# Kernel tuning notes

Hardware: AMD Instinct MI355X
Metric: run time of the kernel (lower is better)

The kernel has to match this reference:

```python
import jax, jax.numpy as jnp
import numpy as np

N_NODES = 50000
N_EDGES = 800000
N_REL = 3
N_GRAPHS = 500
EMB = 128
IN_DIM = EMB * 3
HID = 256
N_CLASS = 10
N_SHAPE, N_COLOR, MAX_POS = 8, 8, 128


def rgcn_layer(h, src, dst, etype, W, root, b):
    """PyG RGCNConv with default aggr='mean':
    out[v] = sum_r mean_{(j->v) in E_r} h[j] @ W[r] + h[v] @ root + b
    Aggregate raw features per (dst, relation) bucket, then apply relation matmuls.
    """
    N, R = h.shape[0], W.shape[0]
    seg = dst * R + etype  # combined (node, relation) segment id
    sums = jax.ops.segment_sum(h[src], seg, num_segments=N * R)          # (N*R, d)
    cnt = jax.ops.segment_sum(jnp.ones(seg.shape, h.dtype), seg, num_segments=N * R)
    mean = (sums / jnp.maximum(cnt, 1.0)[:, None]).reshape(N, R, -1)     # (N, R, d)
    return jnp.einsum('nrd,rdh->nh', mean, W) + h @ root + b


def setup_inputs() -> dict:
    key = jax.random.key(0)
    ks = jax.random.split(key, 20)
    f32 = jnp.float32
    inp = {
        's': jax.random.randint(ks[0], (N_NODES,), 0, N_SHAPE),
        'c': jax.random.randint(ks[1], (N_NODES,), 0, N_COLOR),
        'p': jax.random.randint(ks[2], (N_NODES,), 0, MAX_POS),
        'edge_index': jax.random.randint(ks[3], (2, N_EDGES), 0, N_NODES),
        'edge_type': jax.random.randint(ks[4], (N_EDGES,), 0, N_REL),
        'batch': jnp.sort(jax.random.randint(ks[5], (N_NODES,), 0, N_GRAPHS)),
        'shape_emb': jax.random.normal(ks[6], (N_SHAPE, EMB), f32),
        'color_emb': jax.random.normal(ks[7], (N_COLOR, EMB), f32),
        'pos_emb': jax.random.normal(ks[8], (MAX_POS, EMB), f32),
        'W1': jax.random.normal(ks[9], (N_REL, IN_DIM, HID), f32) / np.sqrt(IN_DIM),
        'root1': jax.random.normal(ks[10], (IN_DIM, HID), f32) / np.sqrt(IN_DIM),
        'b1': jnp.zeros((HID,), f32),
        'W2': jax.random.normal(ks[11], (N_REL, HID, HID), f32) / np.sqrt(HID),
        'root2': jax.random.normal(ks[12], (HID, HID), f32) / np.sqrt(HID),
        'b2': jnp.zeros((HID,), f32),
        'lin_w': jax.random.normal(ks[13], (HID, N_CLASS), f32) / np.sqrt(HID),
        'lin_b': jnp.zeros((N_CLASS,), f32),
    }
    return inp


def reference(s, c, p, edge_index, edge_type, batch,
              shape_emb, color_emb, pos_emb,
              W1, root1, b1, W2, root2, b2, lin_w, lin_b):
    src, dst = edge_index[0], edge_index[1]
    h = jnp.concatenate([shape_emb[s], color_emb[c], pos_emb[p]], axis=-1)  # (N, 3*emb)
    h = jax.nn.relu(rgcn_layer(h, src, dst, edge_type, W1, root1, b1))
    h = jax.nn.relu(rgcn_layer(h, src, dst, edge_type, W2, root2, b2))
    # global_mean_pool over graphs
    gsum = jax.ops.segment_sum(h, batch, num_segments=N_GRAPHS)
    gcnt = jax.ops.segment_sum(jnp.ones((h.shape[0],), h.dtype), batch, num_segments=N_GRAPHS)
    pooled = gsum / jnp.maximum(gcnt, 1.0)[:, None]
    return pooled @ lin_w + lin_b
```

## Files before the change

kernel.cpp:

```cpp
#include <hip/hip_runtime.h>
#include <hip/hip_bf16.h>

#define NN 50000
#define NE 800000
#define NR 3
#define NG 500
#define NB (NN * NR)
#define NCLS 10
#define NCMB 8192
#define CHUNK 2048
#define NBLK ((NB + CHUNK - 1) / CHUNK)

#define P1_COMBO   196
#define P1_ZCNT    586
#define P1_ZPOOL   502
#define P1_TAB     576
#define P1_WF      1024
#define P1_TOTAL   (P1_COMBO + P1_ZCNT + P1_ZPOOL + P1_TAB + P1_WF)
#define P2_CNT     3125
#define P2_TB      768
#define P2_TOTAL   (P2_CNT + P2_TB)

typedef __hip_bfloat16 bf16;
typedef __attribute__((ext_vector_type(8))) short short8;
typedef __attribute__((ext_vector_type(4))) short shortx4;
typedef __attribute__((ext_vector_type(4))) float floatx4;

static __device__ __forceinline__ float b2f(bf16 x) { return __bfloat162float(x); }
static __device__ __forceinline__ bf16  f2b(float x) { return __float2bfloat16(x); }
static __device__ __forceinline__ float bs2f(short x) {
    return __bfloat162float(*reinterpret_cast<const bf16*>(&x));
}
static __device__ __forceinline__ short f2bs(float x) {
    bf16 b = __float2bfloat16(x);
    return *reinterpret_cast<const short*>(&b);
}
static __device__ __forceinline__ int rfl(int x) {
    return __builtin_amdgcn_readfirstlane(x);
}

__global__ __launch_bounds__(256) void prep1(const int* __restrict__ s,
                                             const int* __restrict__ c,
                                             const int* __restrict__ p,
                                             const float* __restrict__ se,
                                             const float* __restrict__ ce,
                                             const float* __restrict__ pe,
                                             const float* __restrict__ W1,
                                             const float* __restrict__ root1,
                                             const float* __restrict__ W2,
                                             const float* __restrict__ root2,
                                             int* __restrict__ combo,
                                             unsigned* __restrict__ cnt,
                                             unsigned* __restrict__ poolz,
                                             float* __restrict__ tab,
                                             bf16* __restrict__ Wf) {
    int b = blockIdx.x, t = threadIdx.x;
    if (b < P1_COMBO) {
        int n = b * 256 + t;
        if (n < NN) combo[n] = (s[n] << 10) | (c[n] << 7) | p[n];
        return;
    }
    b -= P1_COMBO;
    if (b < P1_ZCNT) {
        int i = b * 256 + t;
        if (i < NB) cnt[i] = 0u;
        return;
    }
    b -= P1_ZCNT;
    if (b < P1_ZPOOL) {
        int i = b * 256 + t;
        if (i < NG * 256 + NG) poolz[i] = 0u;
        return;
    }
    b -= P1_ZPOOL;
    if (b < P1_TAB) {
        int r = b / 144, row = b % 144;
        const float* A; int segk;
        if (row < 8)       { A = se + row * 128;        segk = 0; }
        else if (row < 16) { A = ce + (row - 8) * 128;  segk = 128; }
        else               { A = pe + (row - 16) * 128; segk = 256; }
        const float* W = (r < 3) ? (W1 + (size_t)r * 384 * 256) : root1;
        float acc = 0.f;
        for (int k = 0; k < 128; ++k)
            acc += A[k] * W[(size_t)(segk + k) * 256 + t];
        tab[((size_t)r * 144 + row) * 256 + t] = acc;
        return;
    }
    b -= P1_TAB;
    {
        int idx = b * 256 + t;
        int j     = idx & 7;
        int lane  = (idx >> 3) & 63;
        int ni    = (idx >> 9) & 3;
        int chunk = (idx >> 11) & 31;
        int colblk = idx >> 16;
        int col = colblk * 64 + ni * 16 + (lane & 15);
        int k   = chunk * 32 + (lane >> 4) * 8 + j;
        float v = (k < 768) ? W2[((size_t)(k >> 8) * 256 + (k & 255)) * 256 + col]
                            : root2[(size_t)(k - 768) * 256 + col];
        Wf[idx] = f2b(v);
    }
}

__global__ __launch_bounds__(256) void prep2(const int* __restrict__ ei,
                                             const int* __restrict__ et,
                                             int* __restrict__ cnt,
                                             const float* __restrict__ tab,
                                             const float* __restrict__ b1,
                                             bf16* __restrict__ tb2) {
    int b = blockIdx.x, t = threadIdx.x;
    if (b < P2_CNT) {
        int e = b * 256 + t;
        if (e < NE) atomicAdd(&cnt[ei[NE + e] * NR + et[e]], 1);
        return;
    }
    b -= P2_CNT;
    if (b < 256) {
        int r = b >> 6, sc = b & 63, si = sc >> 3, ci = sc & 7;
        float v = tab[((size_t)r * 144 + si) * 256 + t]
                + tab[((size_t)r * 144 + 8 + ci) * 256 + t];
        if (r == 3) v += b1[t];
        tb2[(size_t)b * 256 + t] = f2b(v);
    } else {
        int bb = b - 256;
        int r = bb >> 7, pi = bb & 127;
        tb2[(size_t)(256 + bb) * 256 + t] =
            f2b(tab[((size_t)r * 144 + 16 + pi) * 256 + t]);
    }
}

__global__ __launch_bounds__(256) void scan_block_sums(const int* __restrict__ cnt,
                                                       int* __restrict__ bsum) {
    __shared__ int sm[256];
    int b = blockIdx.x, t = threadIdx.x;
    int base = b * CHUNK + t * 8, s = 0;
#pragma unroll
    for (int j = 0; j < 8; ++j) { int i = base + j; if (i < NB) s += cnt[i]; }
    sm[t] = s; __syncthreads();
    for (int st = 128; st; st >>= 1) { if (t < st) sm[t] += sm[t + st]; __syncthreads(); }
    if (!t) bsum[b] = sm[0];
}

__global__ __launch_bounds__(256) void scan_write(const int* __restrict__ cnt,
                                                  const int* __restrict__ bsum,
                                                  int* __restrict__ off,
                                                  int* __restrict__ cursor) {
    int b = blockIdx.x, t = threadIdx.x;
    int bbase = 0;
    for (int i = 0; i < b; ++i) bbase += bsum[i];
    if (b == 0 && t == 0) {
        int tot = 0;
        for (int i = 0; i < NBLK; ++i) tot += bsum[i];
        off[NB] = tot;
    }
    int base = b * CHUNK + t * 8;
    int v[8], ts = 0;
#pragma unroll
    for (int j = 0; j < 8; ++j) { int i = base + j; v[j] = (i < NB) ? cnt[i] : 0; ts += v[j]; }
    int lane = t & 63, wv = t >> 6;
    int incl = ts;
    for (int d = 1; d < 64; d <<= 1) {
        int o = __shfl_up(incl, d, 64);
        if (lane >= d) incl += o;
    }
    __shared__ int wsum[4];
    if (lane == 63) wsum[wv] = incl;
    __syncthreads();
    int wbase = 0;
    for (int w = 0; w < wv; ++w) wbase += wsum[w];
    int run = bbase + wbase + incl - ts;
#pragma unroll
    for (int j = 0; j < 8; ++j) {
        int i = base + j;
        if (i < NB) { off[i] = run; cursor[i] = run; }
        run += v[j];
    }
}

__global__ __launch_bounds__(256) void scatter_edges(const int* __restrict__ ei,
                                                     const int* __restrict__ et,
                                                     const int* __restrict__ combo,
                                                     int* __restrict__ cursor,
                                                     unsigned* __restrict__ esc) {
    int e = blockIdx.x * 256 + threadIdx.x;
    if (e >= NE) return;
    int b = ei[NE + e] * NR + et[e];
    int pos = atomicAdd(&cursor[b], 1);
    int s = ei[e];
    esc[pos] = ((unsigned)s << 13) | (unsigned)combo[s];
}

__global__ __launch_bounds__(256, 4) void l1_fused(const int* __restrict__ off,
                                                   const unsigned* __restrict__ esc,
                                                   const int* __restrict__ combo,
                                                   const bf16* __restrict__ tb2,
                                                   bf16* __restrict__ h1) {
    int wave = threadIdx.x >> 6, lane = threadIdx.x & 63;
    int dst = blockIdx.x * 4 + wave;
    if (dst >= NN) return;
    int l4 = lane * 4;
    int b0 = dst * NR;
    int o0 = rfl(off[b0]),     o1 = rfl(off[b0 + 1]),
        o2 = rfl(off[b0 + 2]), o3 = rfl(off[b0 + 3]);
    float inv0 = (o1 > o0) ? 1.f / (float)(o1 - o0) : 0.f;
    float inv1 = (o2 > o1) ? 1.f / (float)(o2 - o1) : 0.f;
    float inv2 = (o3 > o2) ? 1.f / (float)(o3 - o2) : 0.f;
    int cmbD = rfl(combo[dst]);
    shortx4 rsc = *(const shortx4*)(tb2 + (size_t)(192 + (cmbD >> 7)) * 256 + l4);
    shortx4 rp  = *(const shortx4*)(tb2 + (size_t)(640 + (cmbD & 127)) * 256 + l4);
    float s[4];
#pragma unroll
    for (int i = 0; i < 4; ++i) s[i] = bs2f(rsc[i]) + bs2f(rp[i]);

    for (int jb = o0; jb < o3; jb += 8) {
        shortx4 sc[8], sp[8]; float w[8];
#pragma unroll
        for (int q = 0; q < 8; ++q) {
            int k = jb + q;
            bool g = k < o3;
            int kk = g ? k : o0;
            unsigned e = esc[kk];
            int r = (kk >= o1) + (kk >= o2);
            w[q] = g ? ((k >= o2) ? inv2 : ((k >= o1) ? inv1 : inv0)) : 0.f;
            sc[q] = *(const shortx4*)(tb2 + (size_t)(r * 64 + ((e & 8191) >> 7)) * 256 + l4);
            sp[q] = *(const shortx4*)(tb2 + (size_t)(256 + r * 128 + (e & 127)) * 256 + l4);
        }
#pragma unroll
        for (int q = 0; q < 8; ++q)
#pragma unroll
            for (int i = 0; i < 4; ++i)
                s[i] += (bs2f(sc[q][i]) + bs2f(sp[q][i])) * w[q];
    }
    shortx4 o;
#pragma unroll
    for (int i = 0; i < 4; ++i) o[i] = f2bs(fmaxf(s[i], 0.f));
    *(shortx4*)(h1 + (size_t)dst * 256 + l4) = o;
}

__global__ __launch_bounds__(256, 4) void agg_all(const int* __restrict__ off,
                                                  const unsigned* __restrict__ esc,
                                                  const bf16* __restrict__ h1,
                                                  bf16* __restrict__ hagg) {
    int wave = threadIdx.x >> 6, lane = threadIdx.x & 63;
    int dst = blockIdx.x * 4 + wave;
    if (dst >= NN) return;
    int l4 = lane * 4;
    int b0 = dst * NR;
    int o0 = rfl(off[b0]),     o1 = rfl(off[b0 + 1]),
        o2 = rfl(off[b0 + 2]), o3 = rfl(off[b0 + 3]);
    float s0[4] = {}, s1[4] = {}, s2[4] = {};
    int n = max(o1 - o0, max(o2 - o1, o3 - o2));
    for (int k = 0; k < n; k += 4) {
#pragma unroll
        for (int kk = 0; kk < 4; ++kk) {
            int i0 = o0 + k + kk, i1 = o1 + k + kk, i2 = o2 + k + kk;
            bool g0 = i0 < o1, g1 = i1 < o2, g2 = i2 < o3;
            unsigned e0 = esc[g0 ? i0 : 0];
            unsigned e1 = esc[g1 ? i1 : 0];
            unsigned e2 = esc[g2 ? i2 : 0];
            shortx4 v0 = *(const shortx4*)(h1 + (size_t)(g0 ? (e0 >> 13) : 0) * 256 + l4);
            shortx4 v1 = *(const shortx4*)(h1 + (size_t)(g1 ? (e1 >> 13) : 0) * 256 + l4);
            shortx4 v2 = *(const shortx4*)(h1 + (size_t)(g2 ? (e2 >> 13) : 0) * 256 + l4);
            float m0 = g0 ? 1.f : 0.f, m1 = g1 ? 1.f : 0.f, m2 = g2 ? 1.f : 0.f;
#pragma unroll
            for (int i = 0; i < 4; ++i) {
                s0[i] += bs2f(v0[i]) * m0;
                s1[i] += bs2f(v1[i]) * m1;
                s2[i] += bs2f(v2[i]) * m2;
            }
        }
    }
    float inv0 = (o1 > o0) ? 1.f / (float)(o1 - o0) : 0.f;
    float inv1 = (o2 > o1) ? 1.f / (float)(o2 - o1) : 0.f;
    float inv2 = (o3 > o2) ? 1.f / (float)(o3 - o2) : 0.f;
    shortx4 w0, w1, w2;
#pragma unroll
    for (int i = 0; i < 4; ++i) {
        w0[i] = f2bs(s0[i] * inv0);
        w1[i] = f2bs(s1[i] * inv1);
        w2[i] = f2bs(s2[i] * inv2);
    }
    bf16* hd = hagg + (size_t)dst * 768 + l4;
    *(shortx4*)(hd)       = w0;
    *(shortx4*)(hd + 256) = w1;
    *(shortx4*)(hd + 512) = w2;
}

__global__ __launch_bounds__(256) void gemm_cat(const bf16* __restrict__ hagg,
                                                const bf16* __restrict__ h1,
                                                const bf16* __restrict__ Wf,
                                                const float* __restrict__ bias,
                                                const int* __restrict__ batch,
                                                float* __restrict__ pool,
                                                float* __restrict__ gcnt) {
    __shared__ short lds[4][2][32 * 40];
    const int t = threadIdx.x;
    const int wave = t >> 6, lane = t & 63;
    const int quad = lane >> 4, l16 = lane & 15;
    const int row0 = blockIdx.x * 32;
    const int colblk = wave;
    const int rsub = lane >> 2;
    const int ksub = (lane & 3) * 8;
    short* A0 = lds[wave][0];
    short* A1 = lds[wave][1];

    const int r0 = min(row0 + rsub, NN - 1);
    const int r1 = min(row0 + 16 + rsub, NN - 1);
    const bf16* gA0 = hagg + (size_t)r0 * 768 + ksub;
    const bf16* gA1 = hagg + (size_t)r1 * 768 + ksub;
    const bf16* gH0 = h1 + (size_t)r0 * 256 + ksub;
    const bf16* gH1 = h1 + (size_t)r1 * 256 + ksub;
    const short8* bbase = (const short8*)Wf + (size_t)colblk * 32 * 4 * 64 + lane;

    auto loadA2 = [&](int k0, short8& a0, short8& a1) {
        if (k0 < 768) { a0 = *(const short8*)(gA0 + k0); a1 = *(const short8*)(gA1 + k0); }
        else          { a0 = *(const short8*)(gH0 + k0 - 768); a1 = *(const short8*)(gH1 + k0 - 768); }
    };
    auto loadB = [&](int chunk, short8* bf4) {
        const short8* bp = bbase + (size_t)chunk * 4 * 64;
#pragma unroll
        for (int ni = 0; ni < 4; ++ni) bf4[ni] = bp[ni * 64];
    };

    floatx4 acc[2][4] = {};
    short8 aE0, aE1, bE[4];
    short8 aO0, aO1, bO[4];
    loadA2(0, aE0, aE1);  loadB(0, bE);
    loadA2(32, aO0, aO1); loadB(1, bO);

#pragma unroll
    for (int i = 0; i < 32; i += 2) {
        *(short8*)&A0[rsub * 40 + ksub] = aE0;
        *(short8*)&A0[(16 + rsub) * 40 + ksub] = aE1;
        {
            short8 af0 = *(const short8*)&A0[l16 * 40 + quad * 8];
            short8 af1 = *(const short8*)&A0[(16 + l16) * 40 + quad * 8];
#pragma unroll
            for (int ni = 0; ni < 4; ++ni) {
                acc[0][ni] = __builtin_amdgcn_mfma_f32_16x16x32_bf16(af0, bE[ni], acc[0][ni], 0, 0, 0);
                acc[1][ni] = __builtin_amdgcn_mfma_f32_16x16x32_bf16(af1, bE[ni], acc[1][ni], 0, 0, 0);
            }
        }
        if (i + 2 < 32) { loadA2((i + 2) * 32, aE0, aE1); loadB(i + 2, bE); }
        *(short8*)&A1[rsub * 40 + ksub] = aO0;
        *(short8*)&A1[(16 + rsub) * 40 + ksub] = aO1;
        {
            short8 af0 = *(const short8*)&A1[l16 * 40 + quad * 8];
            short8 af1 = *(const short8*)&A1[(16 + l16) * 40 + quad * 8];
#pragma unroll
            for (int ni = 0; ni < 4; ++ni) {
                acc[0][ni] = __builtin_amdgcn_mfma_f32_16x16x32_bf16(af0, bO[ni], acc[0][ni], 0, 0, 0);
                acc[1][ni] = __builtin_amdgcn_mfma_f32_16x16x32_bf16(af1, bO[ni], acc[1][ni], 0, 0, 0);
            }
        }
        if (i + 3 < 32) { loadA2((i + 3) * 32, aO0, aO1); loadB(i + 3, bO); }
    }

    __syncthreads();
    short* st = &lds[0][0][0];
#pragma unroll
    for (int mi = 0; mi < 2; ++mi) {
#pragma unroll
        for (int ni = 0; ni < 4; ++ni) {
            int n = colblk * 64 + ni * 16 + l16;
            float bn = bias[n];
#pragma unroll
            for (int ii = 0; ii < 4; ++ii) {
                int lrow = mi * 16 + quad * 4 + ii;
                float v = (row0 + lrow < NN) ? fmaxf(acc[mi][ni][ii] + bn, 0.f) : 0.f;
                st[lrow * 260 + n] = f2bs(v);
            }
        }
    }
    __syncthreads();
    int nrows = NN - row0; if (nrows > 32) nrows = 32;
    int curg = batch[row0];
    float a = 0.f, cntf = 0.f;
    for (int rr = 0; rr < nrows; ++rr) {
        int g = batch[row0 + rr];
        if (g != curg) {
            atomicAdd(&pool[(size_t)curg * 256 + t], a);
            if (t == 0) atomicAdd(&gcnt[curg], cntf);
            a = 0.f; cntf = 0.f; curg = g;
        }
        a += bs2f(st[rr * 260 + t]);
        cntf += 1.f;
    }
    atomicAdd(&pool[(size_t)curg * 256 + t], a);
    if (t == 0) atomicAdd(&gcnt[curg], cntf);
}

__global__ __launch_bounds__(256) void final_head(const float* __restrict__ pool,
                                                  const float* __restrict__ gcnt,
                                                  const float* __restrict__ lin_w,
                                                  const float* __restrict__ lin_b,
                                                  float* __restrict__ out) {
    __shared__ float sm[256];
    int g = blockIdx.x, t = threadIdx.x;
    float inv = 1.0f / fmaxf(gcnt[g], 1.0f);
    sm[t] = pool[(size_t)g * 256 + t] * inv;
    __syncthreads();
    if (t < NCLS) {
        float s = lin_b[t];
        for (int d = 0; d < 256; ++d) s += sm[d] * lin_w[d * NCLS + t];
        out[g * NCLS + t] = s;
    }
}

extern "C" void kernel_launch(void* const* d_in, const int* in_sizes, int n_in,
                              void* d_out, int out_size, void* d_ws, size_t ws_size,
                              hipStream_t stream) {
    const int*   s_idx = (const int*)d_in[0];
    const int*   c_idx = (const int*)d_in[1];
    const int*   p_idx = (const int*)d_in[2];
    const int*   ei    = (const int*)d_in[3];
    const int*   et    = (const int*)d_in[4];
    const int*   batch = (const int*)d_in[5];
    const float* se    = (const float*)d_in[6];
    const float* ce    = (const float*)d_in[7];
    const float* pe    = (const float*)d_in[8];
    const float* W1    = (const float*)d_in[9];
    const float* root1 = (const float*)d_in[10];
    const float* b1    = (const float*)d_in[11];
    const float* W2    = (const float*)d_in[12];
    const float* root2 = (const float*)d_in[13];
    const float* b2    = (const float*)d_in[14];
    const float* lin_w = (const float*)d_in[15];
    const float* lin_b = (const float*)d_in[16];
    float* out = (float*)d_out;

    char* w = (char*)d_ws;
    size_t o = 0;
    auto alloc = [&](size_t bytes) -> void* {
        o = (o + 15) & ~(size_t)15;
        void* ptr = w + o;
        o += bytes;
        return ptr;
    };
    bf16*     hagg   = (bf16*)    alloc((size_t)NN * 768 * 2);
    bf16*     h1     = (bf16*)    alloc((size_t)NN * 256 * 2);
    bf16*     tb2    = (bf16*)    alloc((size_t)768 * 256 * 2);
    int*      combo  = (int*)     alloc((size_t)NN * 4);
    unsigned* esc    = (unsigned*)alloc((size_t)NE * 4);
    int*      cnt    = (int*)     alloc((size_t)NB * 4);
    int*      off    = (int*)     alloc((size_t)(NB + 1) * 4);
    int*      cursor = (int*)     alloc((size_t)NB * 4);
    int*      bsum   = (int*)     alloc((size_t)NBLK * 4);
    float*    tab    = (float*)   alloc((size_t)4 * 144 * 256 * 4);
    bf16*     Wf     = (bf16*)    alloc((size_t)256 * 1024 * 2);
    float*    pool   = (float*)   alloc((size_t)NG * 256 * 4);
    float*    gcnt   = (float*)   alloc((size_t)NG * 4);
    (void)ws_size;

    prep1<<<P1_TOTAL, 256, 0, stream>>>(s_idx, c_idx, p_idx, se, ce, pe,
                                        W1, root1, W2, root2,
                                        combo, (unsigned*)cnt, (unsigned*)pool, tab, Wf);
    prep2<<<P2_TOTAL, 256, 0, stream>>>(ei, et, cnt, tab, b1, tb2);
    scan_block_sums<<<NBLK, 256, 0, stream>>>(cnt, bsum);
    scan_write<<<NBLK, 256, 0, stream>>>(cnt, bsum, off, cursor);
    scatter_edges<<<(NE + 255) / 256, 256, 0, stream>>>(ei, et, combo, cursor, esc);
    l1_fused<<<(NN + 3) / 4, 256, 0, stream>>>(off, esc, combo, tb2, h1);
    agg_all<<<(NN + 3) / 4, 256, 0, stream>>>(off, esc, h1, hagg);
    gemm_cat<<<(NN + 31) / 32, 256, 0, stream>>>(hagg, h1, Wf, b2, batch, pool, gcnt);
    final_head<<<NG, 256, 0, stream>>>(pool, gcnt, lin_w, lin_b, out);
}
```

Baseline: 375.4 us.

## Stage layer-1 lookup table slices in LDS and split edges across quarter-waves

Replaces the per-destination layer-1 kernel with one that loads a 64-column slice of the precomputed relation/embedding table (576 rows) into shared memory per block. Each block then handles 128 destinations for one column slice, and the four 16-lane groups of a wave process different edges in parallel before a shuffle reduction. The aim is to turn scattered global/L2 table reads into LDS reads. The cost is a table load per block, LDS capacity limiting occupancy, and edge indices being re-read by four slice blocks.

```diff
diff --git a/kernel.cpp b/kernel.cpp
--- a/kernel.cpp
+++ b/kernel.cpp
@@ -20,6 +20,12 @@
 #define P2_CNT     3125
 #define P2_TB      768
 #define P2_TOTAL   (P2_CNT + P2_TB)
+
+#define L1_DPB     128
+#define L1_DPW     32
+#define L1_ROWS    576
+#define L1_STRIDE  68
+#define L1_CHUNKS  ((NN + L1_DPB - 1) / L1_DPB)
 
 typedef __hip_bfloat16 bf16;
 typedef __attribute__((ext_vector_type(8))) short short8;
@@ -190,51 +196,74 @@
     esc[pos] = ((unsigned)s << 13) | (unsigned)combo[s];
 }
 
-__global__ __launch_bounds__(256, 4) void l1_fused(const int* __restrict__ off,
-                                                   const unsigned* __restrict__ esc,
-                                                   const int* __restrict__ combo,
-                                                   const bf16* __restrict__ tb2,
-                                                   bf16* __restrict__ h1) {
-    int wave = threadIdx.x >> 6, lane = threadIdx.x & 63;
-    int dst = blockIdx.x * 4 + wave;
-    if (dst >= NN) return;
-    int l4 = lane * 4;
-    int b0 = dst * NR;
-    int o0 = rfl(off[b0]),     o1 = rfl(off[b0 + 1]),
-        o2 = rfl(off[b0 + 2]), o3 = rfl(off[b0 + 3]);
-    float inv0 = (o1 > o0) ? 1.f / (float)(o1 - o0) : 0.f;
-    float inv1 = (o2 > o1) ? 1.f / (float)(o2 - o1) : 0.f;
-    float inv2 = (o3 > o2) ? 1.f / (float)(o3 - o2) : 0.f;
-    int cmbD = rfl(combo[dst]);
-    shortx4 rsc = *(const shortx4*)(tb2 + (size_t)(192 + (cmbD >> 7)) * 256 + l4);
-    shortx4 rp  = *(const shortx4*)(tb2 + (size_t)(640 + (cmbD & 127)) * 256 + l4);
-    float s[4];
-#pragma unroll
-    for (int i = 0; i < 4; ++i) s[i] = bs2f(rsc[i]) + bs2f(rp[i]);
-
-    for (int jb = o0; jb < o3; jb += 8) {
-        shortx4 sc[8], sp[8]; float w[8];
-#pragma unroll
-        for (int q = 0; q < 8; ++q) {
-            int k = jb + q;
-            bool g = k < o3;
-            int kk = g ? k : o0;
-            unsigned e = esc[kk];
-            int r = (kk >= o1) + (kk >= o2);
-            w[q] = g ? ((k >= o2) ? inv2 : ((k >= o1) ? inv1 : inv0)) : 0.f;
-            sc[q] = *(const shortx4*)(tb2 + (size_t)(r * 64 + ((e & 8191) >> 7)) * 256 + l4);
-            sp[q] = *(const shortx4*)(tb2 + (size_t)(256 + r * 128 + (e & 127)) * 256 + l4);
-        }
-#pragma unroll
-        for (int q = 0; q < 8; ++q)
+__global__ __launch_bounds__(256) void l1_lds(const int* __restrict__ off,
+                                              const unsigned* __restrict__ esc,
+                                              const int* __restrict__ combo,
+                                              const bf16* __restrict__ tb2,
+                                              bf16* __restrict__ h1) {
+    __shared__ short T[L1_ROWS * L1_STRIDE];
+    const int slice = blockIdx.x & 3;
+    const int chunk = blockIdx.x >> 2;
+    const int t = threadIdx.x;
+
+    for (int i = t; i < L1_ROWS * 16; i += 256) {
+        int row = i >> 4, c = i & 15;
+        int grow = (row < 192) ? row : row + 64;
+        *(shortx4*)&T[row * L1_STRIDE + c * 4] =
+            *(const shortx4*)(tb2 + (size_t)grow * 256 + slice * 64 + c * 4);
+    }
+    __syncthreads();
+
+    const int wave = t >> 6, lane = t & 63;
+    const int q = lane >> 4, l16 = lane & 15;
+    const int dst0 = chunk * L1_DPB + wave * L1_DPW;
+    const int myd = slice * 64 + l16 * 4;
+
+    for (int di = 0; di < L1_DPW; ++di) {
+        int dst = dst0 + di;
+        if (dst >= NN) break;
+        int b0 = dst * NR;
+        int o0 = rfl(off[b0]),     o1 = rfl(off[b0 + 1]),
+            o2 = rfl(off[b0 + 2]), o3 = rfl(off[b0 + 3]);
+        float inv0 = (o1 > o0) ? 1.f / (float)(o1 - o0) : 0.f;
+        float inv1 = (o2 > o1) ? 1.f / (float)(o2 - o1) : 0.f;
+        float inv2 = (o3 > o2) ? 1.f / (float)(o3 - o2) : 0.f;
+        float acc[4] = {};
+        for (int jb = o0; jb < o3; jb += 8) {
+            int ka = jb + q, kb = jb + 4 + q;
+            bool ga = ka < o3, gb = kb < o3;
+            int kka = ga ? ka : o0, kkb = gb ? kb : o0;
+            unsigned ea = esc[kka];
+            unsigned eb = esc[kkb];
+            int ra = (kka >= o1) + (kka >= o2);
+            int rb = (kkb >= o1) + (kkb >= o2);
+            float wa = ga ? ((ka >= o2) ? inv2 : ((ka >= o1) ? inv1 : inv0)) : 0.f;
+            float wb = gb ? ((kb >= o2) ? inv2 : ((kb >= o1) ? inv1 : inv0)) : 0.f;
+            shortx4 sa = *(const shortx4*)&T[(ra * 64 + ((ea & 8191u) >> 7)) * L1_STRIDE + l16 * 4];
+            shortx4 pa = *(const shortx4*)&T[(192 + ra * 128 + (int)(ea & 127u)) * L1_STRIDE + l16 * 4];
+            shortx4 sb = *(const shortx4*)&T[(rb * 64 + ((eb & 8191u) >> 7)) * L1_STRIDE + l16 * 4];
+            shortx4 pb = *(const shortx4*)&T[(192 + rb * 128 + (int)(eb & 127u)) * L1_STRIDE + l16 * 4];
 #pragma unroll
             for (int i = 0; i < 4; ++i)
-                s[i] += (bs2f(sc[q][i]) + bs2f(sp[q][i])) * w[q];
-    }
-    shortx4 o;
-#pragma unroll
-    for (int i = 0; i < 4; ++i) o[i] = f2bs(fmaxf(s[i], 0.f));
-    *(shortx4*)(h1 + (size_t)dst * 256 + l4) = o;
+                acc[i] += (bs2f(sa[i]) + bs2f(pa[i])) * wa
+                        + (bs2f(sb[i]) + bs2f(pb[i])) * wb;
+        }
+#pragma unroll
+        for (int i = 0; i < 4; ++i) {
+            acc[i] += __shfl_xor(acc[i], 16);
+            acc[i] += __shfl_xor(acc[i], 32);
+        }
+        if (q == 0) {
+            int cmbD = rfl(combo[dst]);
+            shortx4 rsc = *(const shortx4*)(tb2 + (size_t)(192 + (cmbD >> 7)) * 256 + myd);
+            shortx4 rp  = *(const shortx4*)(tb2 + (size_t)(640 + (cmbD & 127)) * 256 + myd);
+            shortx4 o;
+#pragma unroll
+            for (int i = 0; i < 4; ++i)
+                o[i] = f2bs(fmaxf(acc[i] + bs2f(rsc[i]) + bs2f(rp[i]), 0.f));
+            *(shortx4*)(h1 + (size_t)dst * 256 + myd) = o;
+        }
+    }
 }
 
 __global__ __launch_bounds__(256, 4) void agg_all(const int* __restrict__ off,
@@ -459,7 +488,7 @@
     scan_block_sums<<<NBLK, 256, 0, stream>>>(cnt, bsum);
     scan_write<<<NBLK, 256, 0, stream>>>(cnt, bsum, off, cursor);
     scatter_edges<<<(NE + 255) / 256, 256, 0, stream>>>(ei, et, combo, cursor, esc);
-    l1_fused<<<(NN + 3) / 4, 256, 0, stream>>>(off, esc, combo, tb2, h1);
+    l1_lds<<<L1_CHUNKS * 4, 256, 0, stream>>>(off, esc, combo, tb2, h1);
     agg_all<<<(NN + 3) / 4, 256, 0, stream>>>(off, esc, h1, hagg);
     gemm_cat<<<(NN + 31) / 32, 256, 0, stream>>>(hagg, h1, Wf, b2, batch, pool, gcnt);
     final_head<<<NG, 256, 0, stream>>>(pool, gcnt, lin_w, lin_b, out);
```

Measured after the change: 518.1 us. 38.0% more time.

## Compute layer-1 as per-node histogram times table via MFMA

Applied to the files above, without the earlier changes.

Layer 1 is rewritten so each block of 64 destination nodes first builds, in shared memory, a byte histogram of (relation, shape-color) and (relation, position) table indices from incoming edges. It then multiplies the mean-weighted histogram by the precomputed 768x256 table with bf16 MFMA instructions. This replaces per-edge gathers of 256-wide table rows with a dense small GEMM. A new prep3 kernel pre-swizzles the table into MFMA-friendly layout. Byte counters can overflow if more than 255 edges hit one bin, and the weights are now rounded to bf16 before the multiply.

```diff
diff --git a/kernel.cpp b/kernel.cpp
--- a/kernel.cpp
+++ b/kernel.cpp
@@ -20,6 +20,10 @@
 #define P2_CNT     3125
 #define P2_TB      768
 #define P2_TOTAL   (P2_CNT + P2_TB)
+
+#define L1_DPB     64
+#define L1_HS      776
+#define L1_BLOCKS  ((NN + L1_DPB - 1) / L1_DPB)
 
 typedef __hip_bfloat16 bf16;
 typedef __attribute__((ext_vector_type(8))) short short8;
@@ -129,6 +133,17 @@
     }
 }
 
+__global__ __launch_bounds__(256) void prep3(const bf16* __restrict__ tb2,
+                                             bf16* __restrict__ tbf) {
+    int idx = blockIdx.x * 256 + threadIdx.x;
+    int j = idx & 7, lane = (idx >> 3) & 63, ni = (idx >> 9) & 3;
+    int rest = idx >> 11;
+    int chunk = rest % 24, colblk = rest / 24;
+    int col = colblk * 64 + ni * 16 + (lane & 15);
+    int k   = chunk * 32 + (lane >> 4) * 8 + j;
+    tbf[idx] = tb2[(size_t)k * 256 + col];
+}
+
 __global__ __launch_bounds__(256) void scan_block_sums(const int* __restrict__ cnt,
                                                        int* __restrict__ bsum) {
     __shared__ int sm[256];
@@ -190,51 +205,108 @@
     esc[pos] = ((unsigned)s << 13) | (unsigned)combo[s];
 }
 
-__global__ __launch_bounds__(256, 4) void l1_fused(const int* __restrict__ off,
-                                                   const unsigned* __restrict__ esc,
-                                                   const int* __restrict__ combo,
-                                                   const bf16* __restrict__ tb2,
-                                                   bf16* __restrict__ h1) {
-    int wave = threadIdx.x >> 6, lane = threadIdx.x & 63;
-    int dst = blockIdx.x * 4 + wave;
-    if (dst >= NN) return;
-    int l4 = lane * 4;
-    int b0 = dst * NR;
-    int o0 = rfl(off[b0]),     o1 = rfl(off[b0 + 1]),
-        o2 = rfl(off[b0 + 2]), o3 = rfl(off[b0 + 3]);
-    float inv0 = (o1 > o0) ? 1.f / (float)(o1 - o0) : 0.f;
-    float inv1 = (o2 > o1) ? 1.f / (float)(o2 - o1) : 0.f;
-    float inv2 = (o3 > o2) ? 1.f / (float)(o3 - o2) : 0.f;
-    int cmbD = rfl(combo[dst]);
-    shortx4 rsc = *(const shortx4*)(tb2 + (size_t)(192 + (cmbD >> 7)) * 256 + l4);
-    shortx4 rp  = *(const shortx4*)(tb2 + (size_t)(640 + (cmbD & 127)) * 256 + l4);
-    float s[4];
-#pragma unroll
-    for (int i = 0; i < 4; ++i) s[i] = bs2f(rsc[i]) + bs2f(rp[i]);
-
-    for (int jb = o0; jb < o3; jb += 8) {
-        shortx4 sc[8], sp[8]; float w[8];
-#pragma unroll
-        for (int q = 0; q < 8; ++q) {
-            int k = jb + q;
-            bool g = k < o3;
-            int kk = g ? k : o0;
-            unsigned e = esc[kk];
-            int r = (kk >= o1) + (kk >= o2);
-            w[q] = g ? ((k >= o2) ? inv2 : ((k >= o1) ? inv1 : inv0)) : 0.f;
-            sc[q] = *(const shortx4*)(tb2 + (size_t)(r * 64 + ((e & 8191) >> 7)) * 256 + l4);
-            sp[q] = *(const shortx4*)(tb2 + (size_t)(256 + r * 128 + (e & 127)) * 256 + l4);
-        }
-#pragma unroll
-        for (int q = 0; q < 8; ++q)
-#pragma unroll
-            for (int i = 0; i < 4; ++i)
-                s[i] += (bs2f(sc[q][i]) + bs2f(sp[q][i])) * w[q];
-    }
-    shortx4 o;
-#pragma unroll
-    for (int i = 0; i < 4; ++i) o[i] = f2bs(fmaxf(s[i], 0.f));
-    *(shortx4*)(h1 + (size_t)dst * 256 + l4) = o;
+__global__ __launch_bounds__(256) void l1_hist(const int* __restrict__ off,
+                                               const unsigned* __restrict__ esc,
+                                               const int* __restrict__ combo,
+                                               const bf16* __restrict__ tbf,
+                                               bf16* __restrict__ h1) {
+    __shared__ __align__(16) unsigned char HIST[L1_DPB * L1_HS];
+    __shared__ int SOFF[193];
+    __shared__ float INV[L1_DPB][4];
+    const int t = threadIdx.x;
+    const int dst0 = blockIdx.x * L1_DPB;
+
+    for (int i = t; i < (L1_DPB * L1_HS) / 4; i += 256)
+        ((unsigned*)HIST)[i] = 0u;
+    for (int i = t; i < 193; i += 256)
+        SOFF[i] = off[min(dst0 * NR + i, NB)];
+    __syncthreads();
+
+    if (t < L1_DPB) {
+        int base = 3 * t;
+#pragma unroll
+        for (int r = 0; r < 3; ++r) {
+            int c = SOFF[base + r + 1] - SOFF[base + r];
+            INV[t][r] = (c > 0) ? 1.f / (float)c : 0.f;
+        }
+        INV[t][3] = 1.f;
+        if (dst0 + t < NN) {
+            int c = combo[dst0 + t];
+            HIST[t * L1_HS + 192 + (c >> 7)] = 1;
+            HIST[t * L1_HS + 640 + (c & 127)] = 1;
+        }
+    }
+    int E0 = SOFF[0], E1 = SOFF[192];
+    for (int e = E0 + t; e < E1; e += 256) {
+        unsigned ev = esc[e];
+        int lo = 0, hi = 191;
+#pragma unroll 1
+        while (lo < hi) {
+            int mid = (lo + hi + 1) >> 1;
+            if (SOFF[mid] <= e) lo = mid; else hi = mid - 1;
+        }
+        int dr = lo / 3, rel = lo - dr * 3;
+        int sc = (int)((ev & 8191u) >> 7), p = (int)(ev & 127u);
+        int a1 = dr * L1_HS + rel * 64 + sc;
+        int a2 = dr * L1_HS + 256 + rel * 128 + p;
+        atomicAdd((unsigned*)&HIST[a1 & ~3], 1u << (8 * (a1 & 3)));
+        atomicAdd((unsigned*)&HIST[a2 & ~3], 1u << (8 * (a2 & 3)));
+    }
+    __syncthreads();
+
+    const int wave = t >> 6, lane = t & 63;
+    const int quad = lane >> 4, l16 = lane & 15;
+    const short8* bb = (const short8*)tbf + (size_t)wave * 24 * 4 * 64 + lane;
+    floatx4 acc[4][4] = {};
+#pragma unroll 4
+    for (int ch = 0; ch < 24; ++ch) {
+        short8 bf_[4];
+        const short8* bp = bb + (size_t)ch * 4 * 64;
+#pragma unroll
+        for (int ni = 0; ni < 4; ++ni) bf_[ni] = bp[ni * 64];
+        int kb = ch * 32 + quad * 8;
+        int iv = (kb < 256) ? (kb >> 6) : ((kb - 256) >> 7);
+#pragma unroll
+        for (int mi = 0; mi < 4; ++mi) {
+            int row = mi * 16 + l16;
+            unsigned hx = *(const unsigned*)&HIST[row * L1_HS + kb];
+            unsigned hy = *(const unsigned*)&HIST[row * L1_HS + kb + 4];
+            float w = INV[row][iv];
+            short8 af;
+            af[0] = f2bs((float)(hx & 0xffu) * w);
+            af[1] = f2bs((float)((hx >> 8) & 0xffu) * w);
+            af[2] = f2bs((float)((hx >> 16) & 0xffu) * w);
+            af[3] = f2bs((float)(hx >> 24) * w);
+            af[4] = f2bs((float)(hy & 0xffu) * w);
+            af[5] = f2bs((float)((hy >> 8) & 0xffu) * w);
+            af[6] = f2bs((float)((hy >> 16) & 0xffu) * w);
+            af[7] = f2bs((float)(hy >> 24) * w);
+#pragma unroll
+            for (int ni = 0; ni < 4; ++ni)
+                acc[mi][ni] = __builtin_amdgcn_mfma_f32_16x16x32_bf16(af, bf_[ni], acc[mi][ni], 0, 0, 0);
+        }
+    }
+
+    __syncthreads();
+    short* st = (short*)HIST;
+#pragma unroll
+    for (int mi = 0; mi < 4; ++mi)
+#pragma unroll
+        for (int ni = 0; ni < 4; ++ni)
+#pragma unroll
+            for (int ii = 0; ii < 4; ++ii) {
+                int row = mi * 16 + quad * 4 + ii;
+                int col = wave * 64 + ni * 16 + l16;
+                st[row * 264 + col] = f2bs(fmaxf(acc[mi][ni][ii], 0.f));
+            }
+    __syncthreads();
+    int row = t >> 2, cb = (t & 3) * 64;
+    if (dst0 + row < NN) {
+#pragma unroll
+        for (int j = 0; j < 8; ++j)
+            *(short8*)(h1 + (size_t)(dst0 + row) * 256 + cb + j * 8) =
+                *(const short8*)&st[row * 264 + cb + j * 8];
+    }
 }
 
 __global__ __launch_bounds__(256, 4) void agg_all(const int* __restrict__ off,
@@ -440,6 +512,7 @@
     bf16*     hagg   = (bf16*)    alloc((size_t)NN * 768 * 2);
     bf16*     h1     = (bf16*)    alloc((size_t)NN * 256 * 2);
     bf16*     tb2    = (bf16*)    alloc((size_t)768 * 256 * 2);
+    bf16*     tbf    = (bf16*)    alloc((size_t)768 * 256 * 2);
     int*      combo  = (int*)     alloc((size_t)NN * 4);
     unsigned* esc    = (unsigned*)alloc((size_t)NE * 4);
     int*      cnt    = (int*)     alloc((size_t)NB * 4);
@@ -456,10 +529,11 @@
                                         W1, root1, W2, root2,
                                         combo, (unsigned*)cnt, (unsigned*)pool, tab, Wf);
     prep2<<<P2_TOTAL, 256, 0, stream>>>(ei, et, cnt, tab, b1, tb2);
+    prep3<<<768, 256, 0, stream>>>(tb2, tbf);
     scan_block_sums<<<NBLK, 256, 0, stream>>>(cnt, bsum);
     scan_write<<<NBLK, 256, 0, stream>>>(cnt, bsum, off, cursor);
     scatter_edges<<<(NE + 255) / 256, 256, 0, stream>>>(ei, et, combo, cursor, esc);
-    l1_fused<<<(NN + 3) / 4, 256, 0, stream>>>(off, esc, combo, tb2, h1);
+    l1_hist<<<L1_BLOCKS, 256, 0, stream>>>(off, esc, combo, tbf, h1);
     agg_all<<<(NN + 3) / 4, 256, 0, stream>>>(off, esc, h1, hagg);
     gemm_cat<<<(NN + 31) / 32, 256, 0, stream>>>(hagg, h1, Wf, b2, batch, pool, gcnt);
     final_head<<<NG, 256, 0, stream>>>(pool, gcnt, lin_w, lin_b, out);
```

Measured after the change: 359.6 us. -4.2%, faster.
